# Kernel tuning notes

Hardware: AMD Instinct MI355X
Metric: run time of the kernel (lower is better)

The kernel has to match this reference:

```python
import jax, jax.numpy as jnp
import numpy as np

PE_SIZE = 16          # sqrt(num_patches=256)
HIDDEN_STRIDE = 2
CUBIC_A = -0.75       # torch bicubic coefficient


def cubic_resize_matrix(in_size, out_size, a=CUBIC_A):
    """(out_size, in_size) weights for torch bicubic, align_corners=False."""
    dst = np.arange(out_size)
    src = (dst + 0.5) * in_size / out_size - 0.5
    x0 = np.floor(src).astype(np.int64)
    W = np.zeros((out_size, in_size), np.float32)
    for k in range(-1, 3):  # 4 taps
        idx = np.clip(x0 + k, 0, in_size - 1)  # border replicate
        d = np.abs(src - (x0 + k))
        w = np.where(d <= 1.0, (a + 2) * d**3 - (a + 3) * d**2 + 1.0,
            np.where(d < 2.0, a * d**3 - 5 * a * d**2 + 8 * a * d - 4 * a, 0.0))
        np.add.at(W, (dst, idx), w.astype(np.float32))
    return W


def setup_inputs() -> dict:
    key = jax.random.key(0)
    k1, k2, k3, k4 = jax.random.split(key, 4)
    n_img, t, h, w = 8, 1, 64, 64
    total = n_img * t * h * w  # 32768 patches
    in_feat, d = 3 * 14 * 14, 1152
    return {
        "pixel_values": jax.random.normal(k1, (total, in_feat), jnp.float32),
        "w_patch": jax.random.normal(k2, (d, in_feat), jnp.float32) * 0.02,
        "b_patch": jax.random.normal(k3, (d,), jnp.float32) * 0.02,
        "pos_table": jax.random.normal(k4, (PE_SIZE * PE_SIZE, d), jnp.float32) * 0.02,
        "grid_thws": jnp.array([[t, h, w]] * n_img, jnp.int64),
    }


def _pos_embed(pos_table, grid):
    """grid: np int array (n_img, 3) -> (sum t*h*w, d) positional embeddings."""
    d = pos_table.shape[-1]
    pe_grid = pos_table.reshape(PE_SIZE, PE_SIZE, d)  # (H, W, d)
    s = HIDDEN_STRIDE
    pieces = []
    for t, h, w in grid:
        Wh = jnp.asarray(cubic_resize_matrix(PE_SIZE, int(h)))
        Ww = jnp.asarray(cubic_resize_matrix(PE_SIZE, int(w)))
        pe = jnp.einsum('hH,wW,HWd->hwd', Wh, Ww, pe_grid)  # (h, w, d)
        # hidden_stride window rearrange: (h,w,d) -> (h/s, w/s, s, s, d)
        pe = pe.reshape(h // s, s, w // s, s, d).transpose(0, 2, 1, 3, 4)
        pe = pe.reshape(h * w, d)
        pe = jnp.tile(pe, (int(t), 1))  # repeat over temporal dim
        pieces.append(pe)
    return jnp.concatenate(pieces, axis=0)


def reference(pixel_values, w_patch, b_patch, pos_table, grid_thws):
    # patch embedding (Linear)
    patch_embeds = pixel_values @ w_patch.T + b_patch  # (N, d)
    grid = np.asarray(grid_thws)  # static shapes per image
    pos = _pos_embed(pos_table, grid)
    return patch_embeds + pos
```

## Files before the change

kernel.cpp:

```cpp
#include <hip/hip_runtime.h>

typedef unsigned short ushort_t;
typedef unsigned int uint_t;

typedef __bf16 bf16x8 __attribute__((ext_vector_type(8)));
typedef float f32x4 __attribute__((ext_vector_type(4)));

#define KK 588
#define KP 608
#define NN 1152
#define MM 32768
#define POSROWS 4096
#define NSTEP 19
#define GRID 2304
#define CHUNKS_PER_ROW 76
#define ACHUNKS (MM * CHUNKS_PER_ROW)
#define ABLOCKS (ACHUNKS / 256)
#define BCHUNKS (NN * CHUNKS_PER_ROW)
#define BBLOCKS ((BCHUNKS + 255) / 256)

#define AS1 __attribute__((address_space(1)))
#define AS3 __attribute__((address_space(3)))


__device__ __forceinline__ void cubic_taps(int dst, float* w, int* idx) {
    const float A = -0.75f;
    float src = (float)dst * 0.25f - 0.25f;
    int x0 = (int)floorf(src);
    #pragma unroll
    for (int k = -1; k <= 2; ++k) {
        int i = x0 + k;
        int ic = i < 0 ? 0 : (i > 15 ? 15 : i);
        float d = fabsf(src - (float)i);
        float wt;
        if (d <= 1.0f)      wt = ((A + 2.0f) * d - (A + 3.0f)) * d * d + 1.0f;
        else if (d < 2.0f)  wt = ((A * d - 5.0f * A) * d + 8.0f * A) * d - 4.0f * A;
        else                wt = 0.0f;
        w[k + 1] = wt;
        idx[k + 1] = ic;
    }
}

__device__ __forceinline__ void cvt_chunk(const float* __restrict__ src,
                                          ushort_t* __restrict__ dst, int c) {
    int row = c / CHUNKS_PER_ROW;
    int k0 = (c - row * CHUNKS_PER_ROW) * 8;
    const float* g = src + (size_t)row * KK + k0;
    bf16x8 v;
    if (k0 + 8 <= KK) {
        f32x4 a = *(const f32x4*)g;
        f32x4 b = *(const f32x4*)(g + 4);
        #pragma unroll
        for (int e = 0; e < 4; ++e) { v[e] = (__bf16)a[e]; v[e + 4] = (__bf16)b[e]; }
    } else {
        #pragma unroll
        for (int e = 0; e < 8; ++e)
            v[e] = (k0 + e < KK) ? (__bf16)g[e] : (__bf16)0.f;
    }
    *(bf16x8*)(dst + (size_t)row * KP + k0) = v;
}


__global__ void prep_kernel(const float* __restrict__ pv, ushort_t* __restrict__ pvb,
                            const float* __restrict__ wp, ushort_t* __restrict__ wb,
                            const float* __restrict__ pt, const float* __restrict__ bias,
                            float* __restrict__ pos) {
    int b = blockIdx.x;
    if (b < ABLOCKS) {
        cvt_chunk(pv, pvb, b * 256 + threadIdx.x);
    } else if (b < ABLOCKS + BBLOCKS) {
        int c = (b - ABLOCKS) * 256 + threadIdx.x;
        if (c < BCHUNKS) cvt_chunk(wp, wb, c);
    } else {
        int n = b - (ABLOCKS + BBLOCKS);
        int h = ((n >> 7) << 1) | ((n >> 1) & 1);
        int w = (((n >> 2) & 31) << 1) | (n & 1);
        float wh[4], ww[4];
        int ih[4], iw[4];
        cubic_taps(h, wh, ih);
        cubic_taps(w, ww, iw);
        const f32x4* pt4 = (const f32x4*)pt;
        const f32x4* bias4 = (const f32x4*)bias;
        for (int j = threadIdx.x; j < NN / 4; j += blockDim.x) {
            f32x4 s = bias4[j];
            #pragma unroll
            for (int a = 0; a < 4; ++a) {
                #pragma unroll
                for (int bq = 0; bq < 4; ++bq) {
                    float wt = wh[a] * ww[bq];
                    f32x4 vv = pt4[(ih[a] * 16 + iw[bq]) * (NN / 4) + j];
                    s.x += wt * vv.x; s.y += wt * vv.y; s.z += wt * vv.z; s.w += wt * vv.w;
                }
            }
            ((f32x4*)pos)[(size_t)n * (NN / 4) + j] = s;
        }
    }
}


__global__ void gemm_kernel(const ushort_t* __restrict__ Abf,
                            const ushort_t* __restrict__ Bbf,
                            const float* __restrict__ pos,
                            float* __restrict__ out) {
    __shared__ __align__(16) ushort_t lA[3][128 * 32];
    __shared__ __align__(16) ushort_t lB[3][128 * 32];

    const int t = threadIdx.x;
    const int lane = t & 63;
    const int lm = lane & 15;
    const int lq = lane >> 4;
    const int wid = t >> 6;
    const int wm = wid >> 1, wn = wid & 1;

    int blk = (int)blockIdx.x;
    int xcd = blk & 7;
    int local = blk >> 3;
    int pp = local / 72;
    int rem = local - pp * 72;
    int nt = rem >> 3;
    int r  = rem & 7;
    int p  = pp * 8 + xcd;
    int mt = r * 32 + p;
    const int bm = mt * 128;
    const int bn = nt * 128;

    f32x4 acc[4][4] = {};

    auto stage = [&](int ks, int buf) {
        const int k0 = ks * 32;
        #pragma unroll
        for (int j = 0; j < 2; ++j) {
            int idx = j * 256 + t;
            int row = idx >> 2;
            int slot = idx & 3;
            int khi = slot ^ ((row >> 1) & 3);
            const ushort_t* gA = Abf + (size_t)(bm + row) * KP + k0 + khi * 8;
            const ushort_t* gB = Bbf + (size_t)(bn + row) * KP + k0 + khi * 8;
            ushort_t* lAp = &lA[buf][(size_t)(idx & ~63) * 8];
            ushort_t* lBp = &lB[buf][(size_t)(idx & ~63) * 8];
            __builtin_amdgcn_global_load_lds(
                (const AS1 void*)gA, (AS3 void*)lAp, 16, 0, 0);
            __builtin_amdgcn_global_load_lds(
                (const AS1 void*)gB, (AS3 void*)lBp, 16, 0, 0);
        }
    };

    stage(0, 0);
    stage(1, 1);

    for (int ks = 0; ks < NSTEP; ++ks) {
        const int cur = ks % 3;

        if (ks + 2 < NSTEP) {
            stage(ks + 2, (ks + 2) % 3);
            asm volatile("s_waitcnt vmcnt(8)" ::: "memory");
        } else if (ks + 1 < NSTEP) {
            asm volatile("s_waitcnt vmcnt(4)" ::: "memory");
        } else {
            asm volatile("s_waitcnt vmcnt(0)" ::: "memory");
        }
        __builtin_amdgcn_s_barrier();
        __builtin_amdgcn_sched_barrier(0);

        bf16x8 af[4], bfr[4];
        #pragma unroll
        for (int mi = 0; mi < 4; ++mi) {
            int row = wm * 64 + mi * 16 + lm;
            int slot = lq ^ ((row >> 1) & 3);
            af[mi] = *(const bf16x8*)(&lA[cur][row * 32 + slot * 8]);
        }
        #pragma unroll
        for (int ni = 0; ni < 4; ++ni) {
            int row = wn * 64 + ni * 16 + lm;
            int slot = lq ^ ((row >> 1) & 3);
            bfr[ni] = *(const bf16x8*)(&lB[cur][row * 32 + slot * 8]);
        }
        #pragma unroll
        for (int mi = 0; mi < 4; ++mi)
            #pragma unroll
            for (int ni = 0; ni < 4; ++ni)
                acc[mi][ni] = __builtin_amdgcn_mfma_f32_16x16x32_bf16(
                    bfr[ni], af[mi], acc[mi][ni], 0, 0, 0);

        asm volatile("s_waitcnt lgkmcnt(0)" ::: "memory");
        __builtin_amdgcn_s_barrier();
    }

    const int M0 = bm + wm * 64;
    const int N0 = bn + wn * 64;
    #pragma unroll
    for (int mi = 0; mi < 4; ++mi) {
        int m = M0 + mi * 16 + lm;
        const float* posrow = pos + (size_t)(m & (POSROWS - 1)) * NN;
        float* outrow = out + (size_t)m * NN;
        #pragma unroll
        for (int ni = 0; ni < 4; ++ni) {
            int nb = N0 + ni * 16 + lq * 4;
            f32x4 pv4 = *(const f32x4*)(posrow + nb);
            f32x4 v = acc[mi][ni];
            v.x += pv4.x; v.y += pv4.y; v.z += pv4.z; v.w += pv4.w;
            *(f32x4*)(outrow + nb) = v;
        }
    }
}


__global__ void fb_kernel(const float* __restrict__ A, const float* __restrict__ W,
                          const float* __restrict__ bias, const float* __restrict__ pt,
                          float* __restrict__ out) {
    __shared__ float sA[16][17], sB[16][17];
    int ty = threadIdx.y, tx = threadIdx.x;
    int row = blockIdx.y * 16 + ty;
    int col = blockIdx.x * 16 + tx;
    float acc = 0.f;
    for (int k0 = 0; k0 < KK; k0 += 16) {
        int ka = k0 + tx;
        sA[ty][tx] = (ka < KK) ? A[(size_t)row * KK + ka] : 0.f;
        sB[ty][tx] = (ka < KK) ? W[(size_t)(blockIdx.x * 16 + ty) * KK + ka] : 0.f;
        __syncthreads();
        #pragma unroll
        for (int kk = 0; kk < 16; ++kk)
            acc += sA[ty][kk] * sB[tx][kk];
        __syncthreads();
    }
    int n = row & (POSROWS - 1);
    int h = ((n >> 7) << 1) | ((n >> 1) & 1);
    int w = (((n >> 2) & 31) << 1) | (n & 1);
    float wh[4], ww[4]; int ih[4], iw[4];
    cubic_taps(h, wh, ih);
    cubic_taps(w, ww, iw);
    float pq = 0.f;
    #pragma unroll
    for (int a = 0; a < 4; ++a) {
        float rs = 0.f;
        #pragma unroll
        for (int b = 0; b < 4; ++b)
            rs += ww[b] * pt[(ih[a] * 16 + iw[b]) * NN + col];
        pq += wh[a] * rs;
    }
    out[(size_t)row * NN + col] = acc + bias[col] + pq;
}


extern "C" void kernel_launch(void* const* d_in, const int* in_sizes, int n_in,
                              void* d_out, int out_size, void* d_ws, size_t ws_size,
                              hipStream_t stream) {
    const float* pv   = (const float*)d_in[0];
    const float* wp   = (const float*)d_in[1];
    const float* bias = (const float*)d_in[2];
    const float* pt   = (const float*)d_in[3];
    float* out = (float*)d_out;

    const size_t pos_bytes = (size_t)POSROWS * NN * 4;
    const size_t pvb_bytes = (size_t)MM * KP * 2;
    const size_t wb_bytes  = (size_t)NN * KP * 2;
    const size_t need = pos_bytes + pvb_bytes + wb_bytes;

    if (ws_size >= need) {
        float* pos = (float*)d_ws;
        ushort_t* pvb = (ushort_t*)((char*)d_ws + pos_bytes);
        ushort_t* wb  = (ushort_t*)((char*)d_ws + pos_bytes + pvb_bytes);

        prep_kernel<<<ABLOCKS + BBLOCKS + POSROWS, 256, 0, stream>>>(
            pv, pvb, wp, wb, pt, bias, pos);
        gemm_kernel<<<GRID, 256, 0, stream>>>(pvb, wb, pos, out);
    } else {
        fb_kernel<<<dim3(NN / 16, MM / 16), dim3(16, 16), 0, stream>>>(pv, wp, bias, pt, out);
    }
}
```

Baseline: 123.8 us.

## Restructure GEMM to 256x128 tiles, 512 threads, K=64 double buffering with ping-pong phases

```diff
diff --git a/kernel.cpp b/kernel.cpp
--- a/kernel.cpp
+++ b/kernel.cpp
@@ -11,8 +11,11 @@
 #define NN 1152
 #define MM 32768
 #define POSROWS 4096
-#define NSTEP 19
-#define GRID 2304
+#define BMT 256
+#define BNT 128
+#define NFULL 9
+#define KTAIL 576
+#define GRID 1152
 #define CHUNKS_PER_ROW 76
 #define ACHUNKS (MM * CHUNKS_PER_ROW)
 #define ABLOCKS (ACHUNKS / 256)
@@ -98,19 +101,28 @@
 }
 
 
-__global__ void gemm_kernel(const ushort_t* __restrict__ Abf,
-                            const ushort_t* __restrict__ Bbf,
-                            const float* __restrict__ pos,
-                            float* __restrict__ out) {
-    __shared__ __align__(16) ushort_t lA[3][128 * 32];
-    __shared__ __align__(16) ushort_t lB[3][128 * 32];
+#define MFMA_(MI,NI,AR,KH) acc[MI][NI] = __builtin_amdgcn_mfma_f32_16x16x32_bf16( \
+    bfr[NI][KH], af[AR][KH], acc[MI][NI], 0, 0, 0);
+#define MFMT_(MI,NI,AR,AH) acc[MI][NI] = __builtin_amdgcn_mfma_f32_16x16x32_bf16( \
+    bfr[NI][0], af[AR][AH], acc[MI][NI], 0, 0, 0);
+
+__global__ __launch_bounds__(512, 2)
+void gemm_kernel(const ushort_t* __restrict__ Abf,
+                 const ushort_t* __restrict__ Bbf,
+                 const float* __restrict__ pos,
+                 float* __restrict__ out) {
+    __shared__ __align__(16) ushort_t lA[2][BMT * 64];
+    __shared__ __align__(16) ushort_t lB[2][BNT * 64];
+    __shared__ __align__(16) ushort_t lAt[BMT * 32];
+    __shared__ __align__(16) ushort_t lBt[BNT * 32];
 
     const int t = threadIdx.x;
     const int lane = t & 63;
     const int lm = lane & 15;
     const int lq = lane >> 4;
     const int wid = t >> 6;
-    const int wm = wid >> 1, wn = wid & 1;
+    const int wm = wid >> 1;
+    const int wn = wid & 1;
 
     int blk = (int)blockIdx.x;
     int xcd = blk & 7;
@@ -120,71 +132,149 @@
     int nt = rem >> 3;
     int r  = rem & 7;
     int p  = pp * 8 + xcd;
-    int mt = r * 32 + p;
-    const int bm = mt * 128;
-    const int bn = nt * 128;
+    int mt = r * 16 + p;
+    const int bm = mt * BMT;
+    const int bn = nt * BNT;
 
     f32x4 acc[4][4] = {};
-
-    auto stage = [&](int ks, int buf) {
-        const int k0 = ks * 32;
+    bf16x8 af[2][2], bfr[4][2];
+
+    auto stageA = [&](int kt, int buf, int part) {
+        #pragma unroll
+        for (int j = 2 * part; j < 2 * part + 2; ++j) {
+            int idx = j * 512 + t;
+            int row = idx >> 3;
+            int s = idx & 7;
+            int c = s ^ (row & 7);
+            const ushort_t* g = Abf + (size_t)(bm + row) * KP + kt * 64 + c * 8;
+            ushort_t* lp = &lA[buf][(idx & ~63) * 8];
+            __builtin_amdgcn_global_load_lds((const AS1 void*)g, (AS3 void*)lp, 16, 0, 0);
+        }
+    };
+    auto stageB = [&](int kt, int buf) {
         #pragma unroll
         for (int j = 0; j < 2; ++j) {
-            int idx = j * 256 + t;
+            int idx = j * 512 + t;
+            int row = idx >> 3;
+            int s = idx & 7;
+            int c = s ^ (row & 7);
+            const ushort_t* g = Bbf + (size_t)(bn + row) * KP + kt * 64 + c * 8;
+            ushort_t* lp = &lB[buf][(idx & ~63) * 8];
+            __builtin_amdgcn_global_load_lds((const AS1 void*)g, (AS3 void*)lp, 16, 0, 0);
+        }
+    };
+    auto stageAtail = [&]() {
+        #pragma unroll
+        for (int j = 0; j < 2; ++j) {
+            int idx = j * 512 + t;
             int row = idx >> 2;
-            int slot = idx & 3;
-            int khi = slot ^ ((row >> 1) & 3);
-            const ushort_t* gA = Abf + (size_t)(bm + row) * KP + k0 + khi * 8;
-            const ushort_t* gB = Bbf + (size_t)(bn + row) * KP + k0 + khi * 8;
-            ushort_t* lAp = &lA[buf][(size_t)(idx & ~63) * 8];
-            ushort_t* lBp = &lB[buf][(size_t)(idx & ~63) * 8];
-            __builtin_amdgcn_global_load_lds(
-                (const AS1 void*)gA, (AS3 void*)lAp, 16, 0, 0);
-            __builtin_amdgcn_global_load_lds(
-                (const AS1 void*)gB, (AS3 void*)lBp, 16, 0, 0);
-        }
-    };
-
-    stage(0, 0);
-    stage(1, 1);
-
-    for (int ks = 0; ks < NSTEP; ++ks) {
-        const int cur = ks % 3;
-
-        if (ks + 2 < NSTEP) {
-            stage(ks + 2, (ks + 2) % 3);
-            asm volatile("s_waitcnt vmcnt(8)" ::: "memory");
-        } else if (ks + 1 < NSTEP) {
-            asm volatile("s_waitcnt vmcnt(4)" ::: "memory");
-        } else {
-            asm volatile("s_waitcnt vmcnt(0)" ::: "memory");
-        }
-        __builtin_amdgcn_s_barrier();
-        __builtin_amdgcn_sched_barrier(0);
-
-        bf16x8 af[4], bfr[4];
-        #pragma unroll
-        for (int mi = 0; mi < 4; ++mi) {
-            int row = wm * 64 + mi * 16 + lm;
-            int slot = lq ^ ((row >> 1) & 3);
-            af[mi] = *(const bf16x8*)(&lA[cur][row * 32 + slot * 8]);
-        }
-        #pragma unroll
-        for (int ni = 0; ni < 4; ++ni) {
-            int row = wn * 64 + ni * 16 + lm;
-            int slot = lq ^ ((row >> 1) & 3);
-            bfr[ni] = *(const bf16x8*)(&lB[cur][row * 32 + slot * 8]);
-        }
-        #pragma unroll
-        for (int mi = 0; mi < 4; ++mi)
-            #pragma unroll
-            for (int ni = 0; ni < 4; ++ni)
-                acc[mi][ni] = __builtin_amdgcn_mfma_f32_16x16x32_bf16(
-                    bfr[ni], af[mi], acc[mi][ni], 0, 0, 0);
-
+            int s = idx & 3;
+            int c = s ^ ((row >> 1) & 3);
+            const ushort_t* g = Abf + (size_t)(bm + row) * KP + KTAIL + c * 8;
+            ushort_t* lp = &lAt[(idx & ~63) * 8];
+            __builtin_amdgcn_global_load_lds((const AS1 void*)g, (AS3 void*)lp, 16, 0, 0);
+        }
+    };
+    auto stageBtail = [&]() {
+        int idx = t;
+        int row = idx >> 2;
+        int s = idx & 3;
+        int c = s ^ ((row >> 1) & 3);
+        const ushort_t* g = Bbf + (size_t)(bn + row) * KP + KTAIL + c * 8;
+        ushort_t* lp = &lBt[(idx & ~63) * 8];
+        __builtin_amdgcn_global_load_lds((const AS1 void*)g, (AS3 void*)lp, 16, 0, 0);
+    };
+
+    auto rdA = [&](int buf, int mi, int kh) -> bf16x8 {
+        int row = wm * 64 + mi * 16 + lm;
+        int slot = ((kh << 2) | lq) ^ (row & 7);
+        return *(const bf16x8*)(&lA[buf][row * 64 + slot * 8]);
+    };
+    auto rdB = [&](int buf, int ni, int kh) -> bf16x8 {
+        int row = wn * 64 + ni * 16 + lm;
+        int slot = ((kh << 2) | lq) ^ (row & 7);
+        return *(const bf16x8*)(&lB[buf][row * 64 + slot * 8]);
+    };
+    auto rdAt = [&](int mi) -> bf16x8 {
+        int row = wm * 64 + mi * 16 + lm;
+        int slot = lq ^ ((row >> 1) & 3);
+        return *(const bf16x8*)(&lAt[row * 32 + slot * 8]);
+    };
+    auto rdBt = [&](int ni) -> bf16x8 {
+        int row = wn * 64 + ni * 16 + lm;
+        int slot = lq ^ ((row >> 1) & 3);
+        return *(const bf16x8*)(&lBt[row * 32 + slot * 8]);
+    };
+
+    stageA(0, 0, 0); stageA(0, 0, 1); stageB(0, 0);
+
+    for (int kt = 0; kt < NFULL; ++kt) {
+        const int cur = kt & 1, nxt = cur ^ 1;
+        const bool last = (kt == NFULL - 1);
+
+        if (!last) stageA(kt + 1, nxt, 0); else stageAtail();
+        asm volatile("s_waitcnt vmcnt(2)" ::: "memory");
+        __builtin_amdgcn_s_barrier();
+        __builtin_amdgcn_sched_barrier(0);
+
+        af[0][0] = rdA(cur, 0, 0); af[0][1] = rdA(cur, 0, 1);
+        af[1][0] = rdA(cur, 1, 0); af[1][1] = rdA(cur, 1, 1);
+        bfr[0][0] = rdB(cur, 0, 0); bfr[0][1] = rdB(cur, 0, 1);
+        bfr[1][0] = rdB(cur, 1, 0); bfr[1][1] = rdB(cur, 1, 1);
+        if (!last) stageA(kt + 1, nxt, 1); else stageBtail();
         asm volatile("s_waitcnt lgkmcnt(0)" ::: "memory");
-        __builtin_amdgcn_s_barrier();
-    }
+        __builtin_amdgcn_sched_barrier(0);
+        __builtin_amdgcn_s_setprio(1);
+        MFMA_(0,0,0,0) MFMA_(0,0,0,1) MFMA_(0,1,0,0) MFMA_(0,1,0,1)
+        MFMA_(1,0,1,0) MFMA_(1,0,1,1) MFMA_(1,1,1,0) MFMA_(1,1,1,1)
+        __builtin_amdgcn_s_setprio(0);
+        __builtin_amdgcn_sched_barrier(0);
+        __builtin_amdgcn_s_barrier();
+
+        bfr[2][0] = rdB(cur, 2, 0); bfr[2][1] = rdB(cur, 2, 1);
+        bfr[3][0] = rdB(cur, 3, 0); bfr[3][1] = rdB(cur, 3, 1);
+        if (!last) stageB(kt + 1, nxt);
+        asm volatile("s_waitcnt lgkmcnt(0)" ::: "memory");
+        __builtin_amdgcn_sched_barrier(0);
+        __builtin_amdgcn_s_setprio(1);
+        MFMA_(0,2,0,0) MFMA_(0,2,0,1) MFMA_(0,3,0,0) MFMA_(0,3,0,1)
+        MFMA_(1,2,1,0) MFMA_(1,2,1,1) MFMA_(1,3,1,0) MFMA_(1,3,1,1)
+        __builtin_amdgcn_s_setprio(0);
+        __builtin_amdgcn_sched_barrier(0);
+        __builtin_amdgcn_s_barrier();
+
+        af[0][0] = rdA(cur, 2, 0); af[0][1] = rdA(cur, 2, 1);
+        af[1][0] = rdA(cur, 3, 0); af[1][1] = rdA(cur, 3, 1);
+        asm volatile("s_waitcnt lgkmcnt(0)" ::: "memory");
+        __builtin_amdgcn_sched_barrier(0);
+        __builtin_amdgcn_s_setprio(1);
+        MFMA_(2,0,0,0) MFMA_(2,0,0,1) MFMA_(2,1,0,0) MFMA_(2,1,0,1)
+        MFMA_(3,0,1,0) MFMA_(3,0,1,1) MFMA_(3,1,1,0) MFMA_(3,1,1,1)
+        __builtin_amdgcn_s_setprio(0);
+        __builtin_amdgcn_sched_barrier(0);
+        __builtin_amdgcn_s_barrier();
+
+        __builtin_amdgcn_s_setprio(1);
+        MFMA_(2,2,0,0) MFMA_(2,2,0,1) MFMA_(2,3,0,0) MFMA_(2,3,0,1)
+        MFMA_(3,2,1,0) MFMA_(3,2,1,1) MFMA_(3,3,1,0) MFMA_(3,3,1,1)
+        __builtin_amdgcn_s_setprio(0);
+        __builtin_amdgcn_sched_barrier(0);
+        __builtin_amdgcn_s_barrier();
+    }
+
+    asm volatile("s_waitcnt vmcnt(0)" ::: "memory");
+    __builtin_amdgcn_s_barrier();
+    __builtin_amdgcn_sched_barrier(0);
+    af[0][0] = rdAt(0); af[0][1] = rdAt(1); af[1][0] = rdAt(2); af[1][1] = rdAt(3);
+    bfr[0][0] = rdBt(0); bfr[1][0] = rdBt(1); bfr[2][0] = rdBt(2); bfr[3][0] = rdBt(3);
+    asm volatile("s_waitcnt lgkmcnt(0)" ::: "memory");
+    __builtin_amdgcn_sched_barrier(0);
+    __builtin_amdgcn_s_setprio(1);
+    MFMT_(0,0,0,0) MFMT_(0,1,0,0) MFMT_(0,2,0,0) MFMT_(0,3,0,0)
+    MFMT_(1,0,0,1) MFMT_(1,1,0,1) MFMT_(1,2,0,1) MFMT_(1,3,0,1)
+    MFMT_(2,0,1,0) MFMT_(2,1,1,0) MFMT_(2,2,1,0) MFMT_(2,3,1,0)
+    MFMT_(3,0,1,1) MFMT_(3,1,1,1) MFMT_(3,2,1,1) MFMT_(3,3,1,1)
+    __builtin_amdgcn_s_setprio(0);
 
     const int M0 = bm + wm * 64;
     const int N0 = bn + wn * 64;
@@ -263,7 +353,7 @@
 
         prep_kernel<<<ABLOCKS + BBLOCKS + POSROWS, 256, 0, stream>>>(
             pv, pvb, wp, wb, pt, bias, pos);
-        gemm_kernel<<<GRID, 256, 0, stream>>>(pvb, wb, pos, out);
+        gemm_kernel<<<GRID, 512, 0, stream>>>(pvb, wb, pos, out);
     } else {
         fb_kernel<<<dim3(NN / 16, MM / 16), dim3(16, 16), 0, stream>>>(pv, wp, bias, pt, out);
     }
```

New measurement: 139.0 us. 12.2% more time.
